# Performance work log

Measured on AMD Instinct MI355X. Metric: run time of the kernel, lower is better.

Reference implementation:

```python
import jax, jax.numpy as jnp
import numpy as np

D_MODEL = 1024
NUM_HEADS = 16
D_K = D_MODEL // NUM_HEADS
THETA = 10000.0
B, S = 4, 2048


def _rope(x, theta=THETA):
    # x: [b, n, s, d_k]; interleaved pair rotation with base theta
    d = x.shape[-1]
    s = x.shape[-2]
    inv_freq = theta ** (-jnp.arange(0, d, 2, dtype=jnp.float32) / d)  # [d/2]
    pos = jnp.arange(s, dtype=jnp.float32)
    ang = pos[:, None] * inv_freq[None, :]          # [s, d/2]
    cos, sin = jnp.cos(ang), jnp.sin(ang)           # broadcast over b, n
    x1 = x[..., 0::2]
    x2 = x[..., 1::2]
    r1 = x1 * cos - x2 * sin
    r2 = x1 * sin + x2 * cos
    out = jnp.stack([r1, r2], axis=-1).reshape(x.shape)
    return out.astype(x.dtype)


def setup_inputs() -> dict:
    key = jax.random.key(0)
    ks = jax.random.split(key, 5)
    scale = 1.0 / np.sqrt(D_MODEL)
    return {
        "x": jax.random.normal(ks[0], (B, S, D_MODEL), dtype=jnp.float32),
        "W_q": jax.random.normal(ks[1], (D_MODEL, D_MODEL), dtype=jnp.float32) * scale,
        "W_k": jax.random.normal(ks[2], (D_MODEL, D_MODEL), dtype=jnp.float32) * scale,
        "W_v": jax.random.normal(ks[3], (D_MODEL, D_MODEL), dtype=jnp.float32) * scale,
        "W_o": jax.random.normal(ks[4], (D_MODEL, D_MODEL), dtype=jnp.float32) * scale,
    }


def reference(x, W_q, W_k, W_v, W_o):
    b, s, _ = x.shape
    # QKV projections (Linear stores weight as [out, in]; y = x @ W.T)
    q = jnp.einsum("bsd,ed->bse", x, W_q).reshape(b, s, NUM_HEADS, D_K).transpose(0, 2, 1, 3)
    k = jnp.einsum("bsd,ed->bse", x, W_k).reshape(b, s, NUM_HEADS, D_K).transpose(0, 2, 1, 3)
    v = jnp.einsum("bsd,ed->bse", x, W_v).reshape(b, s, NUM_HEADS, D_K).transpose(0, 2, 1, 3)
    q = _rope(q)
    k = _rope(k)
    scale = 1.0 / jnp.sqrt(jnp.asarray(D_K, dtype=x.dtype))
    scores = jnp.einsum("bnqd,bnkd->bnqk", q, k) * scale  # [b,n,s,s]
    causal = jnp.tril(jnp.ones((s, s), dtype=bool))
    scores = jnp.where(causal, scores, jnp.asarray(-jnp.inf, dtype=scores.dtype))
    attn = jax.nn.softmax(scores, axis=-1)
    out = jnp.einsum("bnqk,bnkd->bnqd", attn, v)          # [b,n,s,d_k]
    out = out.transpose(0, 2, 1, 3).reshape(b, s, D_MODEL)
    return jnp.einsum("bsd,ed->bse", out, W_o)
```

## Files before the change

kernel.cpp:

```cpp
#include <hip/hip_runtime.h>

#define AS1 __attribute__((address_space(1)))
#define AS3 __attribute__((address_space(3)))

typedef short short8 __attribute__((ext_vector_type(8)));
typedef float f32x4 __attribute__((ext_vector_type(4)));

#define DM 1024
#define NH 16
#define DKH 64
#define SEQ 2048
#define NB 4
#define ROWS (NB*SEQ)

__device__ __forceinline__ unsigned short f2bf(float x) {
    union { float f; unsigned u; } v; v.f = x;
    unsigned r = v.u + 0x7fffu + ((v.u >> 16) & 1u);
    return (unsigned short)(r >> 16);
}
__device__ __forceinline__ float bf2f(unsigned short b) {
    union { unsigned u; float f; } v; v.u = ((unsigned)b) << 16;
    return v.f;
}
__device__ __forceinline__ unsigned cvtpk_bf16(float lo, float hi) {
    unsigned r;
    asm("v_cvt_pk_bf16_f32 %0, %1, %2" : "=v"(r) : "v"(lo), "v"(hi));
    return r;
}

__device__ __forceinline__ void gload_lds16(const void* g, void* l) {
    const AS1 unsigned int* gp = (const AS1 unsigned int*)(unsigned long long)g;
    AS3 unsigned int* lp = (AS3 unsigned int*)(unsigned)(unsigned long long)l;
    __builtin_amdgcn_global_load_lds(gp, lp, 16, 0, 0);
}

__device__ __forceinline__ f32x4 mfma_bf16(short8 a, short8 b, f32x4 c) {
    return __builtin_amdgcn_mfma_f32_16x16x32_bf16(a, b, c, 0, 0, 0);
}

__global__ void __launch_bounds__(256) cast_bf16_kernel(const float* __restrict__ in,
                                                        unsigned short* __restrict__ out, int n4) {
    int i = blockIdx.x * 256 + threadIdx.x;
    if (i >= n4) return;
    float4 v = reinterpret_cast<const float4*>(in)[i];
    ushort4 o;
    o.x = f2bf(v.x); o.y = f2bf(v.y); o.z = f2bf(v.z); o.w = f2bf(v.w);
    reinterpret_cast<ushort4*>(out)[i] = o;
}

__global__ void __launch_bounds__(256) rope_table_kernel(float2* __restrict__ tab) {
    int idx = blockIdx.x * 256 + threadIdx.x;
    int pos = idx >> 5, i = idx & 31;
    float inv = powf(10000.0f, -(float)i * (1.0f / 32.0f));
    float ang = (float)pos * inv;
    float2 cs; cs.x = cosf(ang); cs.y = sinf(ang);
    tab[idx] = cs;
}

__global__ void __launch_bounds__(256) rope_apply_kernel(unsigned short* __restrict__ Q,
                                                         unsigned short* __restrict__ Kb,
                                                         const float2* __restrict__ tab) {
    int idx = blockIdx.x * 256 + threadIdx.x;
    int row = idx >> 7;
    int g = idx & 127;
    int pos = row & (SEQ - 1);
    const float2* tp = tab + pos * 32 + (g & 7) * 4;
    float c0 = tp[0].x, s0 = tp[0].y, c1 = tp[1].x, s1 = tp[1].y;
    float c2 = tp[2].x, s2 = tp[2].y, c3 = tp[3].x, s3 = tp[3].y;
    size_t off = (size_t)row * DM + (size_t)g * 8;
    #pragma unroll
    for (int w = 0; w < 2; ++w) {
        unsigned short* p = (w ? Kb : Q) + off;
        short8 v = *(const short8*)p;
        float e0 = bf2f((unsigned short)v[0]), e1 = bf2f((unsigned short)v[1]);
        float e2 = bf2f((unsigned short)v[2]), e3 = bf2f((unsigned short)v[3]);
        float e4 = bf2f((unsigned short)v[4]), e5 = bf2f((unsigned short)v[5]);
        float e6 = bf2f((unsigned short)v[6]), e7 = bf2f((unsigned short)v[7]);
        short8 o;
        o[0] = (short)f2bf(e0 * c0 - e1 * s0); o[1] = (short)f2bf(e0 * s0 + e1 * c0);
        o[2] = (short)f2bf(e2 * c1 - e3 * s1); o[3] = (short)f2bf(e2 * s1 + e3 * c1);
        o[4] = (short)f2bf(e4 * c2 - e5 * s2); o[5] = (short)f2bf(e4 * s2 + e5 * c2);
        o[6] = (short)f2bf(e6 * c3 - e7 * s3); o[7] = (short)f2bf(e6 * s3 + e7 * c3);
        *(short8*)p = o;
    }
}

__global__ void __launch_bounds__(256) transpose_v_kernel(const unsigned short* __restrict__ V,
                                                          unsigned short* __restrict__ Vt) {
    __shared__ unsigned short T[4096];
    const int tid = threadIdx.x;
    const int s0 = blockIdx.x * 64, bh = blockIdx.y;
    const int b = bh >> 4, h = bh & 15;
    const unsigned short* src = V + (size_t)(b * SEQ + s0) * DM + h * 64;
    #pragma unroll
    for (int i = 0; i < 2; ++i) {
        int r = i * 32 + (tid >> 3), cg = tid & 7;
        short8 v = *(const short8*)(src + (size_t)r * DM + cg * 8);
        *(short8*)(T + r * 64 + ((cg ^ (r >> 3)) << 3)) = v;
    }
    __syncthreads();
    unsigned short* dst = Vt + (size_t)bh * 64 * SEQ + s0;
    #pragma unroll
    for (int i = 0; i < 2; ++i) {
        int d = i * 32 + (tid >> 3), kg = tid & 7;
        int kc = kg >> 2, m = kg & 3;
        short8 o;
        #pragma unroll
        for (int jj = 0; jj < 8; ++jj) {
            int t = 32 * kc + 16 * (jj >> 2) + 4 * m + (jj & 3);
            o[jj] = (short)T[t * 64 + (((d >> 3) ^ (t >> 3)) << 3) + (d & 7)];
        }
        *(short8*)(dst + (size_t)d * SEQ + kg * 8) = o;
    }
}

template <int STORE_F32>
__device__ __forceinline__ void gemm_bt_body(const unsigned short* __restrict__ A,
                                             const unsigned short* __restrict__ Bw,
                                             void* __restrict__ C, int m0, int n0) {
    __shared__ unsigned short S[128 * 128];
    unsigned short* As = S;
    unsigned short* Bs = S + 128 * 64;
    const int tid = threadIdx.x;
    const int lane = tid & 63;
    const int wave = tid >> 6;
    const int wr = wave >> 1, wc = wave & 1;
    const int l15 = lane & 15, l4 = lane >> 4;

    f32x4 acc[4][4];
    #pragma unroll
    for (int m = 0; m < 4; ++m)
        #pragma unroll
        for (int n = 0; n < 4; ++n) { f32x4 z = {0.f, 0.f, 0.f, 0.f}; acc[m][n] = z; }

    const int srow = wave * 8 + (lane >> 3);
    const int gsw = (lane & 7) ^ (srow & 7);
    const unsigned short* Ag = A + (size_t)m0 * DM;
    const unsigned short* Bg = Bw + (size_t)n0 * DM;

    for (int kt = 0; kt < DM; kt += 64) {
        __syncthreads();
        #pragma unroll
        for (int it = 0; it < 4; ++it) {
            int row = it * 32 + srow;
            gload_lds16(Ag + (size_t)row * DM + kt + gsw * 8, (char*)As + (it * 4 + wave) * 1024);
            gload_lds16(Bg + (size_t)row * DM + kt + gsw * 8, (char*)Bs + (it * 4 + wave) * 1024);
        }
        __syncthreads();
        #pragma unroll
        for (int kc = 0; kc < 2; ++kc) {
            short8 af[4], bfr[4];
            #pragma unroll
            for (int m = 0; m < 4; ++m) {
                int row = 64 * wr + 16 * m + l15;
                int off = row * 128 + (((4 * kc + l4) ^ (row & 7)) << 4);
                af[m] = *(const short8*)((const char*)As + off);
            }
            #pragma unroll
            for (int n = 0; n < 4; ++n) {
                int row = 64 * wc + 16 * n + l15;
                int off = row * 128 + (((4 * kc + l4) ^ (row & 7)) << 4);
                bfr[n] = *(const short8*)((const char*)Bs + off);
            }
            #pragma unroll
            for (int m = 0; m < 4; ++m)
                #pragma unroll
                for (int n = 0; n < 4; ++n)
                    acc[m][n] = mfma_bf16(af[m], bfr[n], acc[m][n]);
        }
    }

    if (STORE_F32) {
        int rbase = m0 + 64 * wr + 4 * l4;
        int cbase = n0 + 64 * wc + l15;
        #pragma unroll
        for (int m = 0; m < 4; ++m)
            #pragma unroll
            for (int n = 0; n < 4; ++n) {
                int c = cbase + 16 * n;
                #pragma unroll
                for (int j = 0; j < 4; ++j)
                    ((float*)C)[(size_t)(rbase + 16 * m + j) * DM + c] = acc[m][n][j];
            }
    } else {
        __syncthreads();
        #pragma unroll
        for (int m = 0; m < 4; ++m) {
            int rb = 64 * wr + 16 * m + 4 * l4;
            int xr = ((rb >> 2) & 7) << 3;
            #pragma unroll
            for (int n = 0; n < 4; ++n) {
                int c = (64 * wc + 16 * n + l15) ^ xr;
                #pragma unroll
                for (int j = 0; j < 4; ++j)
                    S[(rb + j) * 128 + c] = f2bf(acc[m][n][j]);
            }
        }
        __syncthreads();
        unsigned short* Cg = (unsigned short*)C + (size_t)m0 * DM + n0;
        #pragma unroll
        for (int r8 = 0; r8 < 8; ++r8) {
            int row = r8 * 16 + (tid >> 4);
            int oc = tid & 15;
            short8 v = *(const short8*)(S + row * 128 + ((oc ^ ((row >> 2) & 7)) << 3));
            *(short8*)(Cg + (size_t)row * DM + oc * 8) = v;
        }
    }
}

__global__ void __launch_bounds__(256) gemm_qkv_kernel(
    const unsigned short* __restrict__ X,
    const unsigned short* __restrict__ Wq, const unsigned short* __restrict__ Wk,
    const unsigned short* __restrict__ Wv,
    unsigned short* __restrict__ Qo, unsigned short* __restrict__ Ko, unsigned short* __restrict__ Vo) {
    int mt = blockIdx.x >> 3, nt = blockIdx.x & 7;
    const unsigned short* W = blockIdx.z == 0 ? Wq : (blockIdx.z == 1 ? Wk : Wv);
    unsigned short* O = blockIdx.z == 0 ? Qo : (blockIdx.z == 1 ? Ko : Vo);
    gemm_bt_body<0>(X, W, O, mt * 128, nt * 128);
}

__global__ void __launch_bounds__(256) gemm_out_kernel(
    const unsigned short* __restrict__ AO, const unsigned short* __restrict__ Wo,
    float* __restrict__ out) {
    int mt = blockIdx.x >> 3, nt = blockIdx.x & 7;
    gemm_bt_body<1>(AO, Wo, out, mt * 128, nt * 128);
}

template <int MODE>
__device__ __forceinline__ void attn_tile(const char* bK, const char* bV,
                                          const short8 (&aq)[2][2], f32x4 (&oacc)[2][4],
                                          float (&mrow)[2], float (&lrow)[2],
                                          int l15, int l4, int qloc) {
    const float CS = 0.125f * 1.44269504088896f;
    f32x4 sac[2][4];
    #pragma unroll
    for (int f = 0; f < 2; ++f)
        #pragma unroll
        for (int n = 0; n < 4; ++n) { f32x4 z = {0.f, 0.f, 0.f, 0.f}; sac[f][n] = z; }

    #pragma unroll
    for (int kc = 0; kc < 2; ++kc)
        #pragma unroll
        for (int n = 0; n < 4; ++n) {
            int row = 16 * n + l15;
            short8 ak = *(const short8*)(bK + row * 128 + (((4 * kc + l4) ^ (row & 7)) << 4));
            if (MODE < 2) sac[0][n] = mfma_bf16(ak, aq[0][kc], sac[0][n]);
            sac[1][n] = mfma_bf16(ak, aq[1][kc], sac[1][n]);
        }

    short8 pb[2][2];
    #pragma unroll
    for (int f = (MODE == 2 ? 1 : 0); f < 2; ++f) {
        const bool dg = (MODE == 1 && f == 0) || (MODE == 2);
        float sv[4][4];
        float tm = -1e30f;
        #pragma unroll
        for (int n = 0; n < 4; ++n)
            #pragma unroll
            for (int j = 0; j < 4; ++j) {
                float s = sac[f][n][j] * CS;
                if (dg && (16 * n + 4 * l4 + j) > qloc) s = -1e30f;
                sv[n][j] = s;
                tm = fmaxf(tm, s);
            }
        tm = fmaxf(tm, __shfl_xor(tm, 16, 64));
        tm = fmaxf(tm, __shfl_xor(tm, 32, 64));
        float nm = fmaxf(mrow[f], tm);
        float al = exp2f(mrow[f] - nm);
        mrow[f] = nm;
        float pj[4][4];
        float sum = 0.f;
        #pragma unroll
        for (int n = 0; n < 4; ++n)
            #pragma unroll
            for (int j = 0; j < 4; ++j) {
                float p = exp2f(sv[n][j] - nm);
                pj[n][j] = p; sum += p;
            }
        sum += __shfl_xor(sum, 16, 64);
        sum += __shfl_xor(sum, 32, 64);
        lrow[f] = lrow[f] * al + sum;
        #pragma unroll
        for (int n = 0; n < 4; ++n) oacc[f][n] *= al;
        #pragma unroll
        for (int kc = 0; kc < 2; ++kc) {
            union { unsigned u[4]; short8 s8; } P;
            P.u[0] = cvtpk_bf16(pj[2 * kc][0], pj[2 * kc][1]);
            P.u[1] = cvtpk_bf16(pj[2 * kc][2], pj[2 * kc][3]);
            P.u[2] = cvtpk_bf16(pj[2 * kc + 1][0], pj[2 * kc + 1][1]);
            P.u[3] = cvtpk_bf16(pj[2 * kc + 1][2], pj[2 * kc + 1][3]);
            pb[f][kc] = P.s8;
        }
    }

    #pragma unroll
    for (int kc = 0; kc < 2; ++kc)
        #pragma unroll
        for (int n = 0; n < 4; ++n) {
            int row = 16 * n + l15;
            short8 av = *(const short8*)(bV + row * 128 + (((4 * kc + l4) ^ (row & 7)) << 4));
            if (MODE < 2) oacc[0][n] = mfma_bf16(av, pb[0][kc], oacc[0][n]);
            oacc[1][n] = mfma_bf16(av, pb[1][kc], oacc[1][n]);
        }
}

__global__ void __launch_bounds__(256) attn_kernel(const unsigned short* __restrict__ Q,
                                                   const unsigned short* __restrict__ K,
                                                   const unsigned short* __restrict__ Vtg,
                                                   unsigned short* __restrict__ O) {
    __shared__ unsigned short smem[16384];

    const int tid = threadIdx.x, lane = tid & 63, wave = tid >> 6;
    const int l15 = lane & 15, l4 = lane >> 4;
    const int bh = blockIdx.x;
    const int qt = gridDim.y - 1 - blockIdx.y;
    const int b = bh >> 4, h = bh & 15;
    const int q0 = qt * 128;
    const int qloc = 16 * wave + l15;
    const int NT = 2 * qt + 2;
    const size_t base = (size_t)b * SEQ * DM + (size_t)h * DKH;
    const unsigned short* Qb = Q + base;
    const unsigned short* Kb = K + base;
    const unsigned short* Vg = Vtg + (size_t)bh * 64 * SEQ;

    short8 aq[2][2];
    #pragma unroll
    for (int f = 0; f < 2; ++f) {
        const unsigned short* p = Qb + (size_t)(q0 + 64 * f + 16 * wave + l15) * DM + 8 * l4;
        aq[f][0] = *(const short8*)p;
        aq[f][1] = *(const short8*)(p + 32);
    }
    asm volatile("s_waitcnt vmcnt(0)" ::: "memory");

    f32x4 oacc[2][4];
    #pragma unroll
    for (int f = 0; f < 2; ++f)
        #pragma unroll
        for (int n = 0; n < 4; ++n) { f32x4 z = {0.f, 0.f, 0.f, 0.f}; oacc[f][n] = z; }
    float mrow[2] = {-1e30f, -1e30f};
    float lrow[2] = {0.f, 0.f};

    const int srow = wave * 8 + (lane >> 3);
    const int gsw = (lane & 7) ^ (srow & 7);
    const unsigned short* kp = Kb + (size_t)srow * DM + gsw * 8;
    const unsigned short* vp = Vg + (size_t)srow * SEQ + gsw * 8;
    char* LD = (char*)smem;

    {
        char* db = LD;
        gload_lds16(kp, db + wave * 1024);
        gload_lds16(kp + 32 * DM, db + 4096 + wave * 1024);
        gload_lds16(vp, db + 8192 + wave * 1024);
        gload_lds16(vp + 32 * SEQ, db + 12288 + wave * 1024);
        kp += 64 * DM; vp += 64;
    }

    for (int t = 0; t < NT; ++t) {
        const char* bK = LD + (t & 1) * 16384;
        const char* bV = bK + 8192;
        if (t + 1 < NT) {
            char* db = LD + ((t + 1) & 1) * 16384;
            gload_lds16(kp, db + wave * 1024);
            gload_lds16(kp + 32 * DM, db + 4096 + wave * 1024);
            gload_lds16(vp, db + 8192 + wave * 1024);
            gload_lds16(vp + 32 * SEQ, db + 12288 + wave * 1024);
            kp += 64 * DM; vp += 64;
            asm volatile("s_waitcnt vmcnt(4)" ::: "memory");
        } else {
            asm volatile("s_waitcnt vmcnt(0)" ::: "memory");
        }
        __builtin_amdgcn_s_barrier();
        if (t < NT - 2)       attn_tile<0>(bK, bV, aq, oacc, mrow, lrow, l15, l4, qloc);
        else if (t == NT - 2) attn_tile<1>(bK, bV, aq, oacc, mrow, lrow, l15, l4, qloc);
        else                  attn_tile<2>(bK, bV, aq, oacc, mrow, lrow, l15, l4, qloc);
        asm volatile("s_waitcnt lgkmcnt(0)" ::: "memory");
        __builtin_amdgcn_s_barrier();
    }

    unsigned short* ep = smem + wave * 2304;
    float inv[2] = {1.f / lrow[0], 1.f / lrow[1]};
    #pragma unroll
    for (int f = 0; f < 2; ++f)
        #pragma unroll
        for (int n = 0; n < 4; ++n)
            #pragma unroll
            for (int j = 0; j < 4; ++j)
                ep[(f * 16 + l15) * 72 + 16 * n + 4 * l4 + j] = f2bf(oacc[f][n][j] * inv[f]);
    __syncthreads();
    unsigned short* Ob = O + base;
    #pragma unroll
    for (int i = 0; i < 4; ++i) {
        int r = i * 8 + (lane >> 3), cg = lane & 7;
        int grow = q0 + 64 * (r >> 4) + 16 * wave + (r & 15);
        *(short8*)(Ob + (size_t)grow * DM + cg * 8) = *(const short8*)(ep + r * 72 + cg * 8);
    }
}

extern "C" void kernel_launch(void* const* d_in, const int* in_sizes, int n_in,
                              void* d_out, int out_size, void* d_ws, size_t ws_size,
                              hipStream_t stream) {
    (void)in_sizes; (void)n_in; (void)out_size; (void)ws_size;
    const float* x  = (const float*)d_in[0];
    const float* Wq = (const float*)d_in[1];
    const float* Wk = (const float*)d_in[2];
    const float* Wv = (const float*)d_in[3];
    const float* Wo = (const float*)d_in[4];
    float* out = (float*)d_out;

    char* ws = (char*)d_ws;
    const size_t MB = 1024 * 1024;
    unsigned short* xb  = (unsigned short*)(ws);
    unsigned short* Vtg = (unsigned short*)(ws);
    unsigned short* wqb = (unsigned short*)(ws + 16 * MB);
    unsigned short* wkb = (unsigned short*)(ws + 18 * MB);
    unsigned short* wvb = (unsigned short*)(ws + 20 * MB);
    unsigned short* wob = (unsigned short*)(ws + 22 * MB);
    unsigned short* Qb  = (unsigned short*)(ws + 24 * MB);
    unsigned short* Kb  = (unsigned short*)(ws + 40 * MB);
    unsigned short* Vb  = (unsigned short*)(ws + 56 * MB);
    unsigned short* AO  = (unsigned short*)(ws + 72 * MB);
    float2* tab = (float2*)(ws + 88 * MB);

    cast_bf16_kernel<<<8192, 256, 0, stream>>>(x, xb, ROWS * DM / 4);
    cast_bf16_kernel<<<1024, 256, 0, stream>>>(Wq, wqb, DM * DM / 4);
    cast_bf16_kernel<<<1024, 256, 0, stream>>>(Wk, wkb, DM * DM / 4);
    cast_bf16_kernel<<<1024, 256, 0, stream>>>(Wv, wvb, DM * DM / 4);
    cast_bf16_kernel<<<1024, 256, 0, stream>>>(Wo, wob, DM * DM / 4);
    rope_table_kernel<<<SEQ * 32 / 256, 256, 0, stream>>>(tab);
    gemm_qkv_kernel<<<dim3(512, 1, 3), 256, 0, stream>>>(xb, wqb, wkb, wvb, Qb, Kb, Vb);
    rope_apply_kernel<<<ROWS * DM / 8 / 256, 256, 0, stream>>>(Qb, Kb, tab);
    transpose_v_kernel<<<dim3(SEQ / 64, NB * NH), 256, 0, stream>>>(Vb, Vtg);
    attn_kernel<<<dim3(NB * NH, SEQ / 128), 256, 0, stream>>>(Qb, Kb, Vtg, AO);
    gemm_out_kernel<<<512, 256, 0, stream>>>(AO, wob, out);
}
```

Baseline: 228.9 us.

## Fuse RoPE into QKV GEMM epilogue and pair causal query tiles per block

RoPE is now applied in the QKV GEMM store epilogue for the Q and K outputs, which removes the separate rope_apply kernel and its read-modify-write pass over Q and K. The attention kernel now has each block process two query tiles, a long one (qt = 15-p) and a short one (qt = p), so causal work is spread evenly across a grid half the previous size. The cost is extra table loads and math in the GEMM epilogue, and half as many attention blocks, which could leave compute units idle.

```diff
diff --git a/kernel.cpp b/kernel.cpp
--- a/kernel.cpp
+++ b/kernel.cpp
@@ -12,6 +12,7 @@
 #define SEQ 2048
 #define NB 4
 #define ROWS (NB*SEQ)
+#define QTILES (SEQ/128)
 
 __device__ __forceinline__ unsigned short f2bf(float x) {
     union { float f; unsigned u; } v; v.f = x;
@@ -57,34 +58,6 @@
     tab[idx] = cs;
 }
 
-__global__ void __launch_bounds__(256) rope_apply_kernel(unsigned short* __restrict__ Q,
-                                                         unsigned short* __restrict__ Kb,
-                                                         const float2* __restrict__ tab) {
-    int idx = blockIdx.x * 256 + threadIdx.x;
-    int row = idx >> 7;
-    int g = idx & 127;
-    int pos = row & (SEQ - 1);
-    const float2* tp = tab + pos * 32 + (g & 7) * 4;
-    float c0 = tp[0].x, s0 = tp[0].y, c1 = tp[1].x, s1 = tp[1].y;
-    float c2 = tp[2].x, s2 = tp[2].y, c3 = tp[3].x, s3 = tp[3].y;
-    size_t off = (size_t)row * DM + (size_t)g * 8;
-    #pragma unroll
-    for (int w = 0; w < 2; ++w) {
-        unsigned short* p = (w ? Kb : Q) + off;
-        short8 v = *(const short8*)p;
-        float e0 = bf2f((unsigned short)v[0]), e1 = bf2f((unsigned short)v[1]);
-        float e2 = bf2f((unsigned short)v[2]), e3 = bf2f((unsigned short)v[3]);
-        float e4 = bf2f((unsigned short)v[4]), e5 = bf2f((unsigned short)v[5]);
-        float e6 = bf2f((unsigned short)v[6]), e7 = bf2f((unsigned short)v[7]);
-        short8 o;
-        o[0] = (short)f2bf(e0 * c0 - e1 * s0); o[1] = (short)f2bf(e0 * s0 + e1 * c0);
-        o[2] = (short)f2bf(e2 * c1 - e3 * s1); o[3] = (short)f2bf(e2 * s1 + e3 * c1);
-        o[4] = (short)f2bf(e4 * c2 - e5 * s2); o[5] = (short)f2bf(e4 * s2 + e5 * c2);
-        o[6] = (short)f2bf(e6 * c3 - e7 * s3); o[7] = (short)f2bf(e6 * s3 + e7 * c3);
-        *(short8*)p = o;
-    }
-}
-
 __global__ void __launch_bounds__(256) transpose_v_kernel(const unsigned short* __restrict__ V,
                                                           unsigned short* __restrict__ Vt) {
     __shared__ unsigned short T[4096];
@@ -117,7 +90,8 @@
 template <int STORE_F32>
 __device__ __forceinline__ void gemm_bt_body(const unsigned short* __restrict__ A,
                                              const unsigned short* __restrict__ Bw,
-                                             void* __restrict__ C, int m0, int n0) {
+                                             void* __restrict__ C, int m0, int n0,
+                                             const float2* __restrict__ tab, int rope) {
     __shared__ unsigned short S[128 * 128];
     unsigned short* As = S;
     unsigned short* Bs = S + 128 * 64;
@@ -203,6 +177,20 @@
             int row = r8 * 16 + (tid >> 4);
             int oc = tid & 15;
             short8 v = *(const short8*)(S + row * 128 + ((oc ^ ((row >> 2) & 7)) << 3));
+            if (rope) {
+                int pos = (m0 + row) & (SEQ - 1);
+                const float2* tp = tab + pos * 32 + (oc & 7) * 4;
+                short8 o;
+                #pragma unroll
+                for (int tt = 0; tt < 4; ++tt) {
+                    float cc = tp[tt].x, ss = tp[tt].y;
+                    float e0 = bf2f((unsigned short)v[2 * tt]);
+                    float e1 = bf2f((unsigned short)v[2 * tt + 1]);
+                    o[2 * tt]     = (short)f2bf(e0 * cc - e1 * ss);
+                    o[2 * tt + 1] = (short)f2bf(e0 * ss + e1 * cc);
+                }
+                v = o;
+            }
             *(short8*)(Cg + (size_t)row * DM + oc * 8) = v;
         }
     }
@@ -212,18 +200,20 @@
     const unsigned short* __restrict__ X,
     const unsigned short* __restrict__ Wq, const unsigned short* __restrict__ Wk,
     const unsigned short* __restrict__ Wv,
-    unsigned short* __restrict__ Qo, unsigned short* __restrict__ Ko, unsigned short* __restrict__ Vo) {
+    unsigned short* __restrict__ Qo, unsigned short* __restrict__ Ko, unsigned short* __restrict__ Vo,
+    const float2* __restrict__ tab) {
     int mt = blockIdx.x >> 3, nt = blockIdx.x & 7;
-    const unsigned short* W = blockIdx.z == 0 ? Wq : (blockIdx.z == 1 ? Wk : Wv);
-    unsigned short* O = blockIdx.z == 0 ? Qo : (blockIdx.z == 1 ? Ko : Vo);
-    gemm_bt_body<0>(X, W, O, mt * 128, nt * 128);
+    int z = blockIdx.z;
+    const unsigned short* W = z == 0 ? Wq : (z == 1 ? Wk : Wv);
+    unsigned short* O = z == 0 ? Qo : (z == 1 ? Ko : Vo);
+    gemm_bt_body<0>(X, W, O, mt * 128, nt * 128, tab, z < 2);
 }
 
 __global__ void __launch_bounds__(256) gemm_out_kernel(
     const unsigned short* __restrict__ AO, const unsigned short* __restrict__ Wo,
     float* __restrict__ out) {
     int mt = blockIdx.x >> 3, nt = blockIdx.x & 7;
-    gemm_bt_body<1>(AO, Wo, out, mt * 128, nt * 128);
+    gemm_bt_body<1>(AO, Wo, out, mt * 128, nt * 128, nullptr, 0);
 }
 
 template <int MODE>
@@ -304,24 +294,17 @@
         }
 }
 
-__global__ void __launch_bounds__(256) attn_kernel(const unsigned short* __restrict__ Q,
-                                                   const unsigned short* __restrict__ K,
-                                                   const unsigned short* __restrict__ Vtg,
-                                                   unsigned short* __restrict__ O) {
-    __shared__ unsigned short smem[16384];
-
-    const int tid = threadIdx.x, lane = tid & 63, wave = tid >> 6;
-    const int l15 = lane & 15, l4 = lane >> 4;
-    const int bh = blockIdx.x;
-    const int qt = gridDim.y - 1 - blockIdx.y;
-    const int b = bh >> 4, h = bh & 15;
+__device__ __forceinline__ void attn_one(const unsigned short* __restrict__ Qb,
+                                         const unsigned short* __restrict__ Kb,
+                                         const unsigned short* __restrict__ Vg,
+                                         unsigned short* __restrict__ Ob,
+                                         unsigned short* smem, int qt,
+                                         int tid, int lane, int wave, int l15, int l4) {
+    __syncthreads();
+
     const int q0 = qt * 128;
     const int qloc = 16 * wave + l15;
     const int NT = 2 * qt + 2;
-    const size_t base = (size_t)b * SEQ * DM + (size_t)h * DKH;
-    const unsigned short* Qb = Q + base;
-    const unsigned short* Kb = K + base;
-    const unsigned short* Vg = Vtg + (size_t)bh * 64 * SEQ;
 
     short8 aq[2][2];
     #pragma unroll
@@ -387,13 +370,33 @@
             for (int j = 0; j < 4; ++j)
                 ep[(f * 16 + l15) * 72 + 16 * n + 4 * l4 + j] = f2bf(oacc[f][n][j] * inv[f]);
     __syncthreads();
-    unsigned short* Ob = O + base;
     #pragma unroll
     for (int i = 0; i < 4; ++i) {
         int r = i * 8 + (lane >> 3), cg = lane & 7;
         int grow = q0 + 64 * (r >> 4) + 16 * wave + (r & 15);
         *(short8*)(Ob + (size_t)grow * DM + cg * 8) = *(const short8*)(ep + r * 72 + cg * 8);
     }
+}
+
+__global__ void __launch_bounds__(256) attn_kernel(const unsigned short* __restrict__ Q,
+                                                   const unsigned short* __restrict__ K,
+                                                   const unsigned short* __restrict__ Vtg,
+                                                   unsigned short* __restrict__ O) {
+    __shared__ unsigned short smem[16384];
+
+    const int tid = threadIdx.x, lane = tid & 63, wave = tid >> 6;
+    const int l15 = lane & 15, l4 = lane >> 4;
+    const int bh = blockIdx.x;
+    const int pp = blockIdx.y;
+    const int b = bh >> 4, h = bh & 15;
+    const size_t base = (size_t)b * SEQ * DM + (size_t)h * DKH;
+    const unsigned short* Qb = Q + base;
+    const unsigned short* Kb = K + base;
+    const unsigned short* Vg = Vtg + (size_t)bh * 64 * SEQ;
+    unsigned short* Ob = O + base;
+
+    attn_one(Qb, Kb, Vg, Ob, smem, QTILES - 1 - pp, tid, lane, wave, l15, l4);
+    attn_one(Qb, Kb, Vg, Ob, smem, pp, tid, lane, wave, l15, l4);
 }
 
 extern "C" void kernel_launch(void* const* d_in, const int* in_sizes, int n_in,
@@ -427,9 +430,8 @@
     cast_bf16_kernel<<<1024, 256, 0, stream>>>(Wv, wvb, DM * DM / 4);
     cast_bf16_kernel<<<1024, 256, 0, stream>>>(Wo, wob, DM * DM / 4);
     rope_table_kernel<<<SEQ * 32 / 256, 256, 0, stream>>>(tab);
-    gemm_qkv_kernel<<<dim3(512, 1, 3), 256, 0, stream>>>(xb, wqb, wkb, wvb, Qb, Kb, Vb);
-    rope_apply_kernel<<<ROWS * DM / 8 / 256, 256, 0, stream>>>(Qb, Kb, tab);
+    gemm_qkv_kernel<<<dim3(512, 1, 3), 256, 0, stream>>>(xb, wqb, wkb, wvb, Qb, Kb, Vb, tab);
     transpose_v_kernel<<<dim3(SEQ / 64, NB * NH), 256, 0, stream>>>(Vb, Vtg);
-    attn_kernel<<<dim3(NB * NH, SEQ / 128), 256, 0, stream>>>(Qb, Kb, Vtg, AO);
+    attn_kernel<<<dim3(NB * NH, QTILES / 2), 256, 0, stream>>>(Qb, Kb, Vtg, AO);
     gemm_out_kernel<<<512, 256, 0, stream>>>(AO, wob, out);
 }
```

Result: faster. 222.0 us (-3.0%).
